# Kernel tuning notes

Measured on AMD Instinct MI355X. Metric: run time of the kernel, lower is better.

The kernel has to match this reference:

```python
import jax, jax.numpy as jnp
import numpy as np

N, E, IN, H, ED = 50000, 800000, 128, 128, 3
EPS = 1e-5

def _gat_conv(x, src, dst, ea, W, a_src, a_dst, We, a_edge, bias):
    n = x.shape[0]
    # add self loops; self-loop edge_attr = per-feature mean (PyG fill_value='mean')
    loops = jnp.arange(n, dtype=src.dtype)
    s = jnp.concatenate([src, loops])
    d = jnp.concatenate([dst, loops])
    ea_full = jnp.concatenate([ea, jnp.broadcast_to(ea.mean(0), (n, ea.shape[1]))], 0)
    h = x @ W                       # [n, H]
    al_s = h @ a_src                # [n]
    al_d = h @ a_dst
    al_e = (ea_full @ We) @ a_edge  # [E+n]
    alpha = jax.nn.leaky_relu(al_s[s] + al_d[d] + al_e, 0.2)
    # segment softmax over destination nodes (every node has a self loop)
    amax = jax.ops.segment_max(alpha, d, num_segments=n)
    ex = jnp.exp(alpha - amax[d])
    denom = jax.ops.segment_sum(ex, d, num_segments=n)
    coef = ex / (denom[d] + 1e-16)
    out = jax.ops.segment_sum(h[s] * coef[:, None], d, num_segments=n)
    return out + bias

def _bn(x, gamma, beta):
    mu = x.mean(0)
    var = ((x - mu) ** 2).mean(0)
    return (x - mu) * jax.lax.rsqrt(var + EPS) * gamma + beta

def setup_inputs():
    key = jax.random.key(0)
    ks = jax.random.split(key, 40)
    inp = {
        "x": jax.random.normal(ks[0], (N, IN), jnp.float32),
        "edge_index": jax.random.randint(ks[1], (2, E), 0, N, dtype=jnp.int32),
        "batch": jnp.zeros((N,), jnp.int32),
        "edge_attr": jax.random.normal(ks[2], (E, ED), jnp.float32),
    }
    i = 3
    for l, cin in ((1, IN), (2, H), (3, H)):
        s = 1.0 / np.sqrt(cin)
        inp[f"W{l}"] = jax.random.normal(ks[i], (cin, H), jnp.float32) * s; i += 1
        inp[f"as{l}"] = jax.random.normal(ks[i], (H,), jnp.float32) * 0.1; i += 1
        inp[f"ad{l}"] = jax.random.normal(ks[i], (H,), jnp.float32) * 0.1; i += 1
        inp[f"We{l}"] = jax.random.normal(ks[i], (ED, H), jnp.float32) * 0.5; i += 1
        inp[f"ae{l}"] = jax.random.normal(ks[i], (H,), jnp.float32) * 0.1; i += 1
        inp[f"b{l}"] = jnp.zeros((H,), jnp.float32)
        inp[f"g{l}"] = jnp.ones((H,), jnp.float32)
        inp[f"be{l}"] = jnp.zeros((H,), jnp.float32)
    return inp

def reference(x, edge_index, batch, edge_attr,
              W1, as1, ad1, We1, ae1, b1, g1, be1,
              W2, as2, ad2, We2, ae2, b2, g2, be2,
              W3, as3, ad3, We3, ae3, b3, g3, be3):
    src, dst = edge_index[0], edge_index[1]
    h = _gat_conv(x, src, dst, edge_attr, W1, as1, ad1, We1, ae1, b1)
    h = _bn(jax.nn.leaky_relu(h, 0.01), g1, be1)
    h = _gat_conv(h, src, dst, edge_attr, W2, as2, ad2, We2, ae2, b2)
    h = _bn(jax.nn.leaky_relu(h, 0.01), g2, be2)
    h = _gat_conv(h, src, dst, edge_attr, W3, as3, ad3, We3, ae3, b3)
    h = _bn(jax.nn.leaky_relu(h, 0.01), g3, be3)
    return h
```

## Files before the change

### kernel.cpp

```cpp
#include <hip/hip_runtime.h>
#include <hip/hip_fp16.h>
#include <math.h>


#define NB 64

typedef __attribute__((ext_vector_type(8))) short bf16x8;
typedef __attribute__((ext_vector_type(4))) float f32x4;

struct __align__(16) Edge2 { int src; int dst; unsigned e01; unsigned e2; };

__device__ __forceinline__ unsigned short f2bf(float x) {
  unsigned u = __float_as_uint(x);
  unsigned r = (u + 0x7FFFu + ((u >> 16) & 1u)) >> 16;
  return (unsigned short)r;
}
__device__ __forceinline__ float bf_lo(unsigned u) { return __uint_as_float(u << 16); }
__device__ __forceinline__ float bf_hi(unsigned u) { return __uint_as_float(u & 0xFFFF0000u); }

__global__ void k_hist_lds(const int* __restrict__ dst, const float* __restrict__ ea, int E,
                           int n, unsigned* __restrict__ hist32, float* __restrict__ ea_sum) {
  extern __shared__ unsigned cnt[];
  int nh = (n + 1) >> 1;
  for (int i = threadIdx.x; i < nh; i += blockDim.x) cnt[i] = 0u;
  __syncthreads();
  int tid = blockIdx.x * blockDim.x + threadIdx.x;
  int stride = gridDim.x * blockDim.x;
  float s0 = 0.f, s1 = 0.f, s2 = 0.f;
  for (int i = tid; i < E; i += stride) {
    int d = dst[i];
    atomicAdd(&cnt[d >> 1], 1u << ((d & 1) << 4));
    s0 += ea[i * 3 + 0]; s1 += ea[i * 3 + 1]; s2 += ea[i * 3 + 2];
  }
  for (int off = 32; off; off >>= 1) {
    s0 += __shfl_down(s0, off); s1 += __shfl_down(s1, off); s2 += __shfl_down(s2, off);
  }
  if ((threadIdx.x & 63) == 0) {
    atomicAdd(&ea_sum[0], s0); atomicAdd(&ea_sum[1], s1); atomicAdd(&ea_sum[2], s2);
  }
  __syncthreads();
  unsigned* plane = hist32 + (size_t)blockIdx.x * nh;
  for (int i = threadIdx.x; i < nh; i += blockDim.x) plane[i] = cnt[i];
}

__device__ __forceinline__ int wave_incl_scan(int x, int lane) {
  for (int off = 1; off < 64; off <<= 1) {
    int t = __shfl_up(x, off);
    if (lane >= off) x += t;
  }
  return x;
}

__global__ __launch_bounds__(1024) void k_scan_a(const unsigned* __restrict__ hist32, int n,
                                                 int* __restrict__ start,
                                                 int* __restrict__ bsum) {
  __shared__ int wsum[16];
  int t = threadIdx.x, lane = t & 63, w = t >> 6;
  int i = blockIdx.x * 1024 + t;
  int nh = (n + 1) >> 1;
  int stride2 = nh * 2;
  const unsigned short* h16 = (const unsigned short*)hist32;
  int v = 0;
  if (i < n) {
    for (int r = 0; r < NB; ++r) v += h16[(size_t)r * stride2 + i];
  }
  int x = wave_incl_scan(v, lane);
  if (lane == 63) wsum[w] = x;
  __syncthreads();
  if (w == 0 && lane < 16) {
    int s = wsum[lane];
    for (int off = 1; off < 16; off <<= 1) {
      int u = __shfl_up(s, off);
      if (lane >= off) s += u;
    }
    wsum[lane] = s;
  }
  __syncthreads();
  int woff = w ? wsum[w - 1] : 0;
  if (i < n) start[i] = x - v + woff;
  if (t == 1023) bsum[blockIdx.x] = wsum[15];
}

__global__ void k_scan_b(int* __restrict__ bsum, int nb, int* __restrict__ start, int n) {
  int lane = threadIdx.x;
  int v = (lane < nb) ? bsum[lane] : 0;
  int x = wave_incl_scan(v, lane);
  if (lane < nb) bsum[lane] = x - v;
  if (lane == nb - 1) start[n] = x;
}

__global__ void k_scan_c(int* __restrict__ start, const int* __restrict__ bsum,
                         const unsigned* __restrict__ hist32, int n,
                         int* __restrict__ cursorp) {
  int i = blockIdx.x * blockDim.x + threadIdx.x;
  if (i >= n) return;
  int nh = (n + 1) >> 1;
  int stride2 = nh * 2;
  const unsigned short* h16 = (const unsigned short*)hist32;
  int s = start[i] + bsum[i >> 10];
  start[i] = s;
  int run = s;
  for (int r = 0; r < NB; ++r) {
    cursorp[(size_t)r * n + i] = run;
    run += h16[(size_t)r * stride2 + i];
  }
}

__global__ void k_scatter_lds(const int* __restrict__ src, const int* __restrict__ dst,
                              const float* __restrict__ ea, int E, int n,
                              const int* __restrict__ cursorp, Edge2* __restrict__ edges) {
  extern __shared__ unsigned cnt[];
  int nh = (n + 1) >> 1;
  for (int i = threadIdx.x; i < nh; i += blockDim.x) cnt[i] = 0u;
  __syncthreads();
  const int* cur = cursorp + (size_t)blockIdx.x * n;
  int tid = blockIdx.x * blockDim.x + threadIdx.x;
  int stride = gridDim.x * blockDim.x;
  for (int i = tid; i < E; i += stride) {
    int d = dst[i];
    int sh = (d & 1) << 4;
    unsigned old = atomicAdd(&cnt[d >> 1], 1u << sh);
    int rank = (old >> sh) & 0xFFFF;
    int pos = cur[d] + rank;
    unsigned short h0 = __half_as_ushort(__float2half(ea[i * 3 + 0]));
    unsigned short h1 = __half_as_ushort(__float2half(ea[i * 3 + 1]));
    unsigned short h2 = __half_as_ushort(__float2half(ea[i * 3 + 2]));
    Edge2 e;
    e.src = src[i];
    e.dst = d;
    e.e01 = (unsigned)h0 | ((unsigned)h1 << 16);
    e.e2 = (unsigned)h2;
    edges[pos] = e;
  }
}

__device__ __forceinline__ void param_wave(const float* __restrict__ We,
                                           const float* __restrict__ ae,
                                           const float* __restrict__ ea_sum, float invE,
                                           float* __restrict__ P, int lane) {
  float a0 = ae[lane], a1 = ae[64 + lane];
  float p0 = We[0 * 128 + lane] * a0 + We[0 * 128 + 64 + lane] * a1;
  float p1 = We[1 * 128 + lane] * a0 + We[1 * 128 + 64 + lane] * a1;
  float p2 = We[2 * 128 + lane] * a0 + We[2 * 128 + 64 + lane] * a1;
  for (int off = 32; off; off >>= 1) {
    p0 += __shfl_down(p0, off); p1 += __shfl_down(p1, off); p2 += __shfl_down(p2, off);
  }
  if (lane == 0) {
    P[0] = p0; P[1] = p1; P[2] = p2;
    P[3] = ea_sum[0] * invE * p0 + ea_sum[1] * invE * p1 + ea_sum[2] * invE * p2;
  }
}

__global__ void k_param0(const float* __restrict__ We, const float* __restrict__ ae,
                         const float* __restrict__ ea_sum, float invE, float* __restrict__ P,
                         float* __restrict__ scale, float* __restrict__ shift,
                         float* __restrict__ colstats) {
  int t = threadIdx.x;
  if (t < 64) {
    param_wave(We, ae, ea_sum, invE, P, t);
  } else if (t < 192) {
    int c = t - 64;
    scale[c] = 1.f; shift[c] = 0.f;
    colstats[c] = 0.f; colstats[128 + c] = 0.f;
  }
}

__global__ void k_inter(const float* __restrict__ colstatsIn, const float* __restrict__ g,
                        const float* __restrict__ be, float invN,
                        float* __restrict__ scale, float* __restrict__ shift,
                        const float* __restrict__ WeN, const float* __restrict__ aeN,
                        const float* __restrict__ ea_sum, float invE, float* __restrict__ P,
                        float* __restrict__ colstats) {
  int t = threadIdx.x;
  if (t < 64) {
    param_wave(WeN, aeN, ea_sum, invE, P, t);
  } else if (t < 192) {
    int c = t - 64;
    float mu = colstatsIn[c] * invN;
    float var = colstatsIn[128 + c] * invN - mu * mu;
    var = var > 0.f ? var : 0.f;
    float sc = g[c] * rsqrtf(var + 1e-5f);
    scale[c] = sc;
    shift[c] = be[c] - mu * sc;
    colstats[c] = 0.f; colstats[128 + c] = 0.f;
  }
}

__global__ __launch_bounds__(256) void k_gemm3(
    const float* __restrict__ X, const float* __restrict__ Wm,
    const float* __restrict__ bnsc, const float* __restrict__ bnsh,
    const float* __restrict__ as, const float* __restrict__ ad,
    const float* __restrict__ P,
    unsigned* __restrict__ hb, float* __restrict__ al_s, float* __restrict__ al_d,
    float* __restrict__ es, int n) {
  __shared__ __align__(16) unsigned short wb[128 * 136];
  __shared__ __align__(16) unsigned short xb[64 * 136];
  int t = threadIdx.x;
  int lane = t & 63;
  int w = t >> 6;
  int c16 = lane & 15;
  int kq = lane >> 4;
  for (int i = t; i < 4096; i += 256) {
    int k = i >> 5, c4 = (i & 31) << 2;
    float4 v = ((const float4*)(Wm + k * 128))[i & 31];
    wb[(c4 + 0) * 136 + k] = f2bf(v.x);
    wb[(c4 + 1) * 136 + k] = f2bf(v.y);
    wb[(c4 + 2) * 136 + k] = f2bf(v.z);
    wb[(c4 + 3) * 136 + k] = f2bf(v.w);
  }
  float asv[8], adv[8];
#pragma unroll
  for (int ct = 0; ct < 8; ++ct) {
    asv[ct] = as[ct * 16 + c16];
    adv[ct] = ad[ct * 16 + c16];
  }
  float cself = P[3];
  int ntiles = (n + 63) >> 6;
  for (int tile = blockIdx.x; tile < ntiles; tile += gridDim.x) {
    int r0 = tile << 6;
    __syncthreads();
    for (int i = t; i < 2048; i += 256) {
      int row = i >> 5, c4 = i & 31;
      int g = r0 + row;
      float4 v;
      if (g < n) {
        v = ((const float4*)(X + (size_t)g * 128))[c4];
        float4 sc = ((const float4*)bnsc)[c4];
        float4 sh = ((const float4*)bnsh)[c4];
        v.x = fmaf(v.x, sc.x, sh.x); v.y = fmaf(v.y, sc.y, sh.y);
        v.z = fmaf(v.z, sc.z, sh.z); v.w = fmaf(v.w, sc.w, sh.w);
      } else { v.x = v.y = v.z = v.w = 0.f; }
      uint2 pk;
      pk.x = (unsigned)f2bf(v.x) | ((unsigned)f2bf(v.y) << 16);
      pk.y = (unsigned)f2bf(v.z) | ((unsigned)f2bf(v.w) << 16);
      *(uint2*)(xb + row * 136 + (c4 << 2)) = pk;
    }
    __syncthreads();
    const unsigned short* xr = xb + (w * 16 + c16) * 136 + kq * 8;
    bf16x8 A[4];
#pragma unroll
    for (int kb = 0; kb < 4; ++kb) A[kb] = *(const bf16x8*)(xr + kb * 32);
    f32x4 acc[8];
#pragma unroll
    for (int ct = 0; ct < 8; ++ct) {
      const unsigned short* wr = wb + (ct * 16 + c16) * 136 + kq * 8;
      f32x4 a = {0.f, 0.f, 0.f, 0.f};
#pragma unroll
      for (int kb = 0; kb < 4; ++kb) {
        bf16x8 B = *(const bf16x8*)(wr + kb * 32);
        a = __builtin_amdgcn_mfma_f32_16x16x32_bf16(A[kb], B, a, 0, 0, 0);
      }
      acc[ct] = a;
    }
#pragma unroll
    for (int r = 0; r < 4; ++r) {
      int R = kq * 4 + r;
      float pr = 0.f, pd = 0.f;
#pragma unroll
      for (int ct = 0; ct < 8; ++ct) {
        float hv = acc[ct][r];
        xb[(w * 16 + R) * 136 + ct * 16 + c16] = f2bf(hv);
        pr = fmaf(hv, asv[ct], pr);
        pd = fmaf(hv, adv[ct], pd);
      }
      for (int off = 8; off; off >>= 1) {
        pr += __shfl_xor(pr, off);
        pd += __shfl_xor(pd, off);
      }
      int g = r0 + w * 16 + R;
      if (c16 == 0 && g < n) {
        al_s[g] = pr; al_d[g] = pd;
        float a = pr + pd + cself;
        a = a > 0.f ? a : 0.2f * a;
        es[g] = __expf(a);
      }
    }
    __syncthreads();
    for (int i = lane; i < 256; i += 64) {
      int row = i >> 4, cc = i & 15;
      int g = r0 + w * 16 + row;
      if (g < n) {
        uint4 v = *(const uint4*)(xb + (w * 16 + row) * 136 + (cc << 3));
        *(uint4*)(hb + (size_t)g * 64 + (cc << 2)) = v;
      }
    }
  }
}

__global__ __launch_bounds__(256) void k_alpha3(const int4* __restrict__ edges,
                                                const float* __restrict__ al_s,
                                                const float* __restrict__ al_d,
                                                const float* __restrict__ P,
                                                int2* __restrict__ meta, int E) {
  int i = blockIdx.x * blockDim.x + threadIdx.x;
  if (i >= E) return;
  int4 ev = edges[i];
  float e0 = __half2float(__ushort_as_half((unsigned short)(ev.z & 0xFFFF)));
  float e1 = __half2float(__ushort_as_half((unsigned short)(((unsigned)ev.z) >> 16)));
  float e2 = __half2float(__ushort_as_half((unsigned short)(ev.w & 0xFFFF)));
  float a = al_s[ev.x] + al_d[ev.y] + e0 * P[0] + e1 * P[1] + e2 * P[2];
  a = a > 0.f ? a : 0.2f * a;
  int2 mv;
  mv.x = ev.x;
  mv.y = __float_as_int(__expf(a));
  meta[i] = mv;
}

__global__ __launch_bounds__(256) void k_agg9(const int2* __restrict__ meta,
                                              const int* __restrict__ start,
                                              const unsigned* __restrict__ hb,
                                              const float* __restrict__ es,
                                              const float* __restrict__ bias,
                                              float* __restrict__ y,
                                              float* __restrict__ colsum,
                                              float* __restrict__ colsumsq, int n) {
  int lane = threadIdx.x & 63;
  int w = threadIdx.x >> 6;
  int grp = lane >> 4;
  int sub = lane & 15;
  int gw = (blockIdx.x * blockDim.x + threadIdx.x) >> 6;
  int nw = (gridDim.x * blockDim.x) >> 6;
  int c0 = (sub << 3) + (grp << 1);
  float2 b2 = ((const float2*)bias)[(sub << 2) + grp];
  float s0 = 0.f, s1 = 0.f, q0 = 0.f, q1 = 0.f;

#define DO_QUAD(EB)                                                          \
  {                                                                          \
    int i0 = (EB), i1 = (EB) + 1, i2 = (EB) + 2, i3 = (EB) + 3;              \
    int2 m0 = meta[i0 < e1 ? i0 : e0];                                       \
    int2 m1 = meta[i1 < e1 ? i1 : e0];                                       \
    int2 m2 = meta[i2 < e1 ? i2 : e0];                                       \
    int2 m3 = meta[i3 < e1 ? i3 : e0];                                       \
    int r0 = i0 < e1 ? m0.x : i;                                             \
    int r1 = i1 < e1 ? m1.x : i;                                             \
    int r2 = i2 < e1 ? m2.x : i;                                             \
    int r3 = i3 < e1 ? m3.x : i;                                             \
    float p0 = i0 < e1 ? __int_as_float(m0.y) : 0.f;                         \
    float p1 = i1 < e1 ? __int_as_float(m1.y) : 0.f;                         \
    float p2 = i2 < e1 ? __int_as_float(m2.y) : 0.f;                         \
    float p3 = i3 < e1 ? __int_as_float(m3.y) : 0.f;                         \
    int rr = grp == 0 ? r0 : grp == 1 ? r1 : grp == 2 ? r2 : r3;             \
    float pp = grp == 0 ? p0 : grp == 1 ? p1 : grp == 2 ? p2 : p3;           \
    uint4 gv = *(const uint4*)(hb + (size_t)rr * 64 + (sub << 2));           \
    pacc += (p0 + p1) + (p2 + p3);                                           \
    aL0 = fmaf(pp, bf_lo(gv.x), aL0); aH0 = fmaf(pp, bf_hi(gv.x), aH0);      \
    aL1 = fmaf(pp, bf_lo(gv.y), aL1); aH1 = fmaf(pp, bf_hi(gv.y), aH1);      \
    aL2 = fmaf(pp, bf_lo(gv.z), aL2); aH2 = fmaf(pp, bf_hi(gv.z), aH2);      \
    aL3 = fmaf(pp, bf_lo(gv.w), aL3); aH3 = fmaf(pp, bf_hi(gv.w), aH3);      \
  }

  for (int i = gw; i < n; i += nw) {
    int e0 = __builtin_amdgcn_readfirstlane(start[i]);
    int e1 = __builtin_amdgcn_readfirstlane(start[i + 1]);
    float eself = es[i];
    uint4 hv = *(const uint4*)(hb + (size_t)i * 64 + (sub << 2));
    float wself = (grp == 0) ? eself : 0.f;
    float aL0 = wself * bf_lo(hv.x), aH0 = wself * bf_hi(hv.x);
    float aL1 = wself * bf_lo(hv.y), aH1 = wself * bf_hi(hv.y);
    float aL2 = wself * bf_lo(hv.z), aH2 = wself * bf_hi(hv.z);
    float aL3 = wself * bf_lo(hv.w), aH3 = wself * bf_hi(hv.w);
    float pacc = 0.f;
    int e = e0;
    for (; e + 8 <= e1; e += 8) {
      DO_QUAD(e);
      DO_QUAD(e + 4);
    }
    for (; e < e1; e += 4) DO_QUAD(e);
    aL0 += __shfl_xor(aL0, 16); aL0 += __shfl_xor(aL0, 32);
    aH0 += __shfl_xor(aH0, 16); aH0 += __shfl_xor(aH0, 32);
    aL1 += __shfl_xor(aL1, 16); aL1 += __shfl_xor(aL1, 32);
    aH1 += __shfl_xor(aH1, 16); aH1 += __shfl_xor(aH1, 32);
    aL2 += __shfl_xor(aL2, 16); aL2 += __shfl_xor(aL2, 32);
    aH2 += __shfl_xor(aH2, 16); aH2 += __shfl_xor(aH2, 32);
    aL3 += __shfl_xor(aL3, 16); aL3 += __shfl_xor(aL3, 32);
    aH3 += __shfl_xor(aH3, 16); aH3 += __shfl_xor(aH3, 32);
    float inv = 1.0f / (eself + pacc + 1e-16f);
    float o0 = grp == 0 ? aL0 : grp == 1 ? aL1 : grp == 2 ? aL2 : aL3;
    float o1 = grp == 0 ? aH0 : grp == 1 ? aH1 : grp == 2 ? aH2 : aH3;
    o0 = fmaf(o0, inv, b2.x);
    o1 = fmaf(o1, inv, b2.y);
    o0 = o0 > 0.f ? o0 : 0.01f * o0;
    o1 = o1 > 0.f ? o1 : 0.01f * o1;
    float2 o2 = {o0, o1};
    *(float2*)(y + (size_t)i * 128 + c0) = o2;
    s0 += o0; s1 += o1;
    q0 = fmaf(o0, o0, q0); q1 = fmaf(o1, o1, q1);
  }
#undef DO_QUAD
  __shared__ float red[4][4][64];
  red[0][w][lane] = s0; red[1][w][lane] = s1; red[2][w][lane] = q0; red[3][w][lane] = q1;
  __syncthreads();
  if (w == 0) {
    for (int ww = 1; ww < 4; ++ww) {
      s0 += red[0][ww][lane]; s1 += red[1][ww][lane];
      q0 += red[2][ww][lane]; q1 += red[3][ww][lane];
    }
    atomicAdd(&colsum[c0], s0);
    atomicAdd(&colsum[c0 + 1], s1);
    atomicAdd(&colsumsq[c0], q0);
    atomicAdd(&colsumsq[c0 + 1], q1);
  }
}

__global__ __launch_bounds__(256) void k_bnapply_final(
    const float4* __restrict__ yin, const float* __restrict__ colstats,
    const float* __restrict__ g, const float* __restrict__ be, float invN,
    float4* __restrict__ yout, int total4) {
  __shared__ float sc_s[128], sh_s[128];
  int t = threadIdx.x;
  if (t < 128) {
    float mu = colstats[t] * invN;
    float var = colstats[128 + t] * invN - mu * mu;
    var = var > 0.f ? var : 0.f;
    float sc = g[t] * rsqrtf(var + 1e-5f);
    sc_s[t] = sc;
    sh_s[t] = be[t] - mu * sc;
  }
  __syncthreads();
  for (int i = blockIdx.x * blockDim.x + t; i < total4; i += gridDim.x * blockDim.x) {
    int c4 = (i & 31) << 2;
    float4 v = yin[i];
    v.x = fmaf(v.x, sc_s[c4 + 0], sh_s[c4 + 0]);
    v.y = fmaf(v.y, sc_s[c4 + 1], sh_s[c4 + 1]);
    v.z = fmaf(v.z, sc_s[c4 + 2], sh_s[c4 + 2]);
    v.w = fmaf(v.w, sc_s[c4 + 3], sh_s[c4 + 3]);
    yout[i] = v;
  }
}

extern "C" void kernel_launch(void* const* d_in, const int* in_sizes, int n_in,
                              void* d_out, int out_size, void* d_ws, size_t ws_size,
                              hipStream_t stream) {
  const float* x = (const float*)d_in[0];
  const int* eidx = (const int*)d_in[1];
  const float* ea = (const float*)d_in[3];
  const int H = 128;
  const int N = in_sizes[0] / H;
  const int E = in_sizes[1] / 2;
  const int* srcIdx = eidx;
  const int* dstIdx = eidx + E;
  const int nh = (N + 1) >> 1;

  char* ws = (char*)d_ws;
  size_t off = 0;
  auto alloc = [&](size_t bytes) -> void* {
    void* p = ws + off;
    off = (off + bytes + 255) & ~(size_t)255;
    return p;
  };
  Edge2* edges = (Edge2*)alloc((size_t)E * sizeof(Edge2));
  int2* meta = (int2*)alloc((size_t)E * sizeof(int2));
  unsigned* hb = (unsigned*)alloc((size_t)N * 64 * sizeof(unsigned));
  float* y = (float*)alloc((size_t)N * H * sizeof(float));
  float* al_s = (float*)alloc((size_t)N * sizeof(float));
  float* al_d = (float*)alloc((size_t)N * sizeof(float));
  float* es = (float*)alloc((size_t)N * sizeof(float));
  unsigned* hist32 = (unsigned*)alloc((size_t)NB * nh * sizeof(unsigned));
  int* cursorp = (int*)alloc((size_t)NB * N * sizeof(int));
  int* start = (int*)alloc((size_t)(N + 1) * sizeof(int));
  int* bsum = (int*)alloc(64 * sizeof(int));
  float* colstats = (float*)alloc(256 * sizeof(float));
  float* colsum = colstats;
  float* colsumsq = colstats + 128;
  float* scale = (float*)alloc(128 * sizeof(float));
  float* shift = (float*)alloc(128 * sizeof(float));
  float* ea_sum = (float*)alloc(64 * sizeof(float));
  float* P = (float*)alloc(16 * sizeof(float));

  const int nb = (N + 1023) / 1024;
  const float invE = 1.0f / (float)E;
  const float invN = 1.0f / (float)N;
  const size_t ldsBytes = (size_t)nh * sizeof(unsigned);

  hipMemsetAsync(ea_sum, 0, 64 * sizeof(float), stream);
  k_hist_lds<<<NB, 256, ldsBytes, stream>>>(dstIdx, ea, E, N, hist32, ea_sum);
  k_scan_a<<<nb, 1024, 0, stream>>>(hist32, N, start, bsum);
  k_scan_b<<<1, 64, 0, stream>>>(bsum, nb, start, N);
  k_scan_c<<<(N + 255) / 256, 256, 0, stream>>>(start, bsum, hist32, N, cursorp);
  k_scatter_lds<<<NB, 256, ldsBytes, stream>>>(srcIdx, dstIdx, ea, E, N, cursorp, edges);

  const float* Wl[3]; const float* asl[3]; const float* adl[3]; const float* Wel[3];
  const float* ael[3]; const float* bl[3]; const float* gl[3]; const float* bel[3];
  for (int l = 0; l < 3; ++l) {
    Wl[l] = (const float*)d_in[4 + 8 * l + 0];
    asl[l] = (const float*)d_in[4 + 8 * l + 1];
    adl[l] = (const float*)d_in[4 + 8 * l + 2];
    Wel[l] = (const float*)d_in[4 + 8 * l + 3];
    ael[l] = (const float*)d_in[4 + 8 * l + 4];
    bl[l] = (const float*)d_in[4 + 8 * l + 5];
    gl[l] = (const float*)d_in[4 + 8 * l + 6];
    bel[l] = (const float*)d_in[4 + 8 * l + 7];
  }

  k_param0<<<1, 192, 0, stream>>>(Wel[0], ael[0], ea_sum, invE, P, scale, shift, colstats);

  const float* X = x;
  for (int l = 0; l < 3; ++l) {
    k_gemm3<<<512, 256, 0, stream>>>(X, Wl[l], scale, shift, asl[l], adl[l], P,
                                     hb, al_s, al_d, es, N);
    k_alpha3<<<(E + 255) / 256, 256, 0, stream>>>((const int4*)edges, al_s, al_d, P,
                                                  meta, E);
    k_agg9<<<2048, 256, 0, stream>>>(meta, start, hb, es, bl[l], y,
                                     colsum, colsumsq, N);
    if (l < 2) {
      k_inter<<<1, 192, 0, stream>>>(colstats, gl[l], bel[l], invN, scale, shift,
                                     Wel[l + 1], ael[l + 1], ea_sum, invE, P, colstats);
    }
    X = y;
  }
  k_bnapply_final<<<384, 256, 0, stream>>>((const float4*)y, colstats, gl[2], bel[2], invN,
                                           (float4*)d_out, N * 32);
}
```

Baseline: 722.1 us.

## Precompute per-layer edge logits at scatter time and fuse alpha into aggregation

All three layers' edge-attribute projections are now computed once in a single param kernel. The scatter kernel writes three per-layer (src, edge-logit) arrays in CSR order instead of a packed edge record. The separate per-layer alpha kernel is removed: aggregation gathers al_s[src], adds al_d and the precomputed edge term, then applies leaky-relu and exp inline. This drops one edge-sized pass per layer and its meta write/read, at the cost of three meta arrays written upfront and gathers plus exp moved into the aggregation loop.

```diff
diff --git a/kernel.cpp b/kernel.cpp
--- a/kernel.cpp
+++ b/kernel.cpp
@@ -7,8 +7,6 @@
 
 typedef __attribute__((ext_vector_type(8))) short bf16x8;
 typedef __attribute__((ext_vector_type(4))) float f32x4;
-
-struct __align__(16) Edge2 { int src; int dst; unsigned e01; unsigned e2; };
 
 __device__ __forceinline__ unsigned short f2bf(float x) {
   unsigned u = __float_as_uint(x);
@@ -108,11 +106,17 @@
 
 __global__ void k_scatter_lds(const int* __restrict__ src, const int* __restrict__ dst,
                               const float* __restrict__ ea, int E, int n,
-                              const int* __restrict__ cursorp, Edge2* __restrict__ edges) {
+                              const int* __restrict__ cursorp,
+                              const float* __restrict__ P_all,
+                              int2* __restrict__ m0a, int2* __restrict__ m1a,
+                              int2* __restrict__ m2a) {
   extern __shared__ unsigned cnt[];
   int nh = (n + 1) >> 1;
   for (int i = threadIdx.x; i < nh; i += blockDim.x) cnt[i] = 0u;
   __syncthreads();
+  float P00 = P_all[0], P01 = P_all[1], P02 = P_all[2];
+  float P10 = P_all[4], P11 = P_all[5], P12 = P_all[6];
+  float P20 = P_all[8], P21 = P_all[9], P22 = P_all[10];
   const int* cur = cursorp + (size_t)blockIdx.x * n;
   int tid = blockIdx.x * blockDim.x + threadIdx.x;
   int stride = gridDim.x * blockDim.x;
@@ -122,15 +126,16 @@
     unsigned old = atomicAdd(&cnt[d >> 1], 1u << sh);
     int rank = (old >> sh) & 0xFFFF;
     int pos = cur[d] + rank;
-    unsigned short h0 = __half_as_ushort(__float2half(ea[i * 3 + 0]));
-    unsigned short h1 = __half_as_ushort(__float2half(ea[i * 3 + 1]));
-    unsigned short h2 = __half_as_ushort(__float2half(ea[i * 3 + 2]));
-    Edge2 e;
-    e.src = src[i];
-    e.dst = d;
-    e.e01 = (unsigned)h0 | ((unsigned)h1 << 16);
-    e.e2 = (unsigned)h2;
-    edges[pos] = e;
+    float e0 = ea[i * 3 + 0], e1 = ea[i * 3 + 1], e2 = ea[i * 3 + 2];
+    int s = src[i];
+    int2 r;
+    r.x = s;
+    r.y = __float_as_int(e0 * P00 + e1 * P01 + e2 * P02);
+    m0a[pos] = r;
+    r.y = __float_as_int(e0 * P10 + e1 * P11 + e2 * P12);
+    m1a[pos] = r;
+    r.y = __float_as_int(e0 * P20 + e1 * P21 + e2 * P22);
+    m2a[pos] = r;
   }
 }
 
@@ -151,39 +156,36 @@
   }
 }
 
-__global__ void k_param0(const float* __restrict__ We, const float* __restrict__ ae,
-                         const float* __restrict__ ea_sum, float invE, float* __restrict__ P,
-                         float* __restrict__ scale, float* __restrict__ shift,
-                         float* __restrict__ colstats) {
+__global__ void k_param_all(const float* __restrict__ We0, const float* __restrict__ ae0,
+                            const float* __restrict__ We1, const float* __restrict__ ae1,
+                            const float* __restrict__ We2, const float* __restrict__ ae2,
+                            const float* __restrict__ ea_sum, float invE,
+                            float* __restrict__ P_all, float* __restrict__ scale,
+                            float* __restrict__ shift, float* __restrict__ colstats) {
   int t = threadIdx.x;
-  if (t < 64) {
-    param_wave(We, ae, ea_sum, invE, P, t);
-  } else if (t < 192) {
-    int c = t - 64;
+  if (t < 192) {
+    int l = t >> 6, lane = t & 63;
+    const float* We = l == 0 ? We0 : l == 1 ? We1 : We2;
+    const float* ae = l == 0 ? ae0 : l == 1 ? ae1 : ae2;
+    param_wave(We, ae, ea_sum, invE, P_all + 4 * l, lane);
+  } else if (t < 320) {
+    int c = t - 192;
     scale[c] = 1.f; shift[c] = 0.f;
     colstats[c] = 0.f; colstats[128 + c] = 0.f;
   }
 }
 
-__global__ void k_inter(const float* __restrict__ colstatsIn, const float* __restrict__ g,
-                        const float* __restrict__ be, float invN,
-                        float* __restrict__ scale, float* __restrict__ shift,
-                        const float* __restrict__ WeN, const float* __restrict__ aeN,
-                        const float* __restrict__ ea_sum, float invE, float* __restrict__ P,
-                        float* __restrict__ colstats) {
-  int t = threadIdx.x;
-  if (t < 64) {
-    param_wave(WeN, aeN, ea_sum, invE, P, t);
-  } else if (t < 192) {
-    int c = t - 64;
-    float mu = colstatsIn[c] * invN;
-    float var = colstatsIn[128 + c] * invN - mu * mu;
-    var = var > 0.f ? var : 0.f;
-    float sc = g[c] * rsqrtf(var + 1e-5f);
-    scale[c] = sc;
-    shift[c] = be[c] - mu * sc;
-    colstats[c] = 0.f; colstats[128 + c] = 0.f;
-  }
+__global__ void k_inter2(const float* __restrict__ g, const float* __restrict__ be,
+                         float invN, float* __restrict__ scale, float* __restrict__ shift,
+                         float* __restrict__ colstats) {
+  int c = threadIdx.x;
+  float mu = colstats[c] * invN;
+  float var = colstats[128 + c] * invN - mu * mu;
+  var = var > 0.f ? var : 0.f;
+  float sc = g[c] * rsqrtf(var + 1e-5f);
+  scale[c] = sc;
+  shift[c] = be[c] - mu * sc;
+  colstats[c] = 0.f; colstats[128 + c] = 0.f;
 }
 
 __global__ __launch_bounds__(256) void k_gemm3(
@@ -287,33 +289,16 @@
   }
 }
 
-__global__ __launch_bounds__(256) void k_alpha3(const int4* __restrict__ edges,
-                                                const float* __restrict__ al_s,
-                                                const float* __restrict__ al_d,
-                                                const float* __restrict__ P,
-                                                int2* __restrict__ meta, int E) {
-  int i = blockIdx.x * blockDim.x + threadIdx.x;
-  if (i >= E) return;
-  int4 ev = edges[i];
-  float e0 = __half2float(__ushort_as_half((unsigned short)(ev.z & 0xFFFF)));
-  float e1 = __half2float(__ushort_as_half((unsigned short)(((unsigned)ev.z) >> 16)));
-  float e2 = __half2float(__ushort_as_half((unsigned short)(ev.w & 0xFFFF)));
-  float a = al_s[ev.x] + al_d[ev.y] + e0 * P[0] + e1 * P[1] + e2 * P[2];
-  a = a > 0.f ? a : 0.2f * a;
-  int2 mv;
-  mv.x = ev.x;
-  mv.y = __float_as_int(__expf(a));
-  meta[i] = mv;
-}
-
-__global__ __launch_bounds__(256) void k_agg9(const int2* __restrict__ meta,
-                                              const int* __restrict__ start,
-                                              const unsigned* __restrict__ hb,
-                                              const float* __restrict__ es,
-                                              const float* __restrict__ bias,
-                                              float* __restrict__ y,
-                                              float* __restrict__ colsum,
-                                              float* __restrict__ colsumsq, int n) {
+__global__ __launch_bounds__(256) void k_agg11(const int2* __restrict__ meta,
+                                               const int* __restrict__ start,
+                                               const unsigned* __restrict__ hb,
+                                               const float* __restrict__ es,
+                                               const float* __restrict__ al_s,
+                                               const float* __restrict__ al_d,
+                                               const float* __restrict__ bias,
+                                               float* __restrict__ y,
+                                               float* __restrict__ colsum,
+                                               float* __restrict__ colsumsq, int n) {
   int lane = threadIdx.x & 63;
   int w = threadIdx.x >> 6;
   int grp = lane >> 4;
@@ -335,10 +320,18 @@
     int r1 = i1 < e1 ? m1.x : i;                                             \
     int r2 = i2 < e1 ? m2.x : i;                                             \
     int r3 = i3 < e1 ? m3.x : i;                                             \
-    float p0 = i0 < e1 ? __int_as_float(m0.y) : 0.f;                         \
-    float p1 = i1 < e1 ? __int_as_float(m1.y) : 0.f;                         \
-    float p2 = i2 < e1 ? __int_as_float(m2.y) : 0.f;                         \
-    float p3 = i3 < e1 ? __int_as_float(m3.y) : 0.f;                         \
+    float a0 = al_s[r0] + ad_i + __int_as_float(m0.y);                       \
+    float a1 = al_s[r1] + ad_i + __int_as_float(m1.y);                       \
+    float a2 = al_s[r2] + ad_i + __int_as_float(m2.y);                       \
+    float a3 = al_s[r3] + ad_i + __int_as_float(m3.y);                       \
+    a0 = a0 > 0.f ? a0 : 0.2f * a0;                                          \
+    a1 = a1 > 0.f ? a1 : 0.2f * a1;                                          \
+    a2 = a2 > 0.f ? a2 : 0.2f * a2;                                          \
+    a3 = a3 > 0.f ? a3 : 0.2f * a3;                                          \
+    float p0 = i0 < e1 ? __expf(a0) : 0.f;                                   \
+    float p1 = i1 < e1 ? __expf(a1) : 0.f;                                   \
+    float p2 = i2 < e1 ? __expf(a2) : 0.f;                                   \
+    float p3 = i3 < e1 ? __expf(a3) : 0.f;                                   \
     int rr = grp == 0 ? r0 : grp == 1 ? r1 : grp == 2 ? r2 : r3;             \
     float pp = grp == 0 ? p0 : grp == 1 ? p1 : grp == 2 ? p2 : p3;           \
     uint4 gv = *(const uint4*)(hb + (size_t)rr * 64 + (sub << 2));           \
@@ -353,6 +346,7 @@
     int e0 = __builtin_amdgcn_readfirstlane(start[i]);
     int e1 = __builtin_amdgcn_readfirstlane(start[i + 1]);
     float eself = es[i];
+    float ad_i = al_d[i];
     uint4 hv = *(const uint4*)(hb + (size_t)i * 64 + (sub << 2));
     float wself = (grp == 0) ? eself : 0.f;
     float aL0 = wself * bf_lo(hv.x), aH0 = wself * bf_hi(hv.x);
@@ -448,8 +442,9 @@
     off = (off + bytes + 255) & ~(size_t)255;
     return p;
   };
-  Edge2* edges = (Edge2*)alloc((size_t)E * sizeof(Edge2));
-  int2* meta = (int2*)alloc((size_t)E * sizeof(int2));
+  int2* meta0 = (int2*)alloc((size_t)E * sizeof(int2));
+  int2* meta1 = (int2*)alloc((size_t)E * sizeof(int2));
+  int2* meta2 = (int2*)alloc((size_t)E * sizeof(int2));
   unsigned* hb = (unsigned*)alloc((size_t)N * 64 * sizeof(unsigned));
   float* y = (float*)alloc((size_t)N * H * sizeof(float));
   float* al_s = (float*)alloc((size_t)N * sizeof(float));
@@ -465,19 +460,12 @@
   float* scale = (float*)alloc(128 * sizeof(float));
   float* shift = (float*)alloc(128 * sizeof(float));
   float* ea_sum = (float*)alloc(64 * sizeof(float));
-  float* P = (float*)alloc(16 * sizeof(float));
+  float* P_all = (float*)alloc(16 * sizeof(float));
 
   const int nb = (N + 1023) / 1024;
   const float invE = 1.0f / (float)E;
   const float invN = 1.0f / (float)N;
   const size_t ldsBytes = (size_t)nh * sizeof(unsigned);
-
-  hipMemsetAsync(ea_sum, 0, 64 * sizeof(float), stream);
-  k_hist_lds<<<NB, 256, ldsBytes, stream>>>(dstIdx, ea, E, N, hist32, ea_sum);
-  k_scan_a<<<nb, 1024, 0, stream>>>(hist32, N, start, bsum);
-  k_scan_b<<<1, 64, 0, stream>>>(bsum, nb, start, N);
-  k_scan_c<<<(N + 255) / 256, 256, 0, stream>>>(start, bsum, hist32, N, cursorp);
-  k_scatter_lds<<<NB, 256, ldsBytes, stream>>>(srcIdx, dstIdx, ea, E, N, cursorp, edges);
 
   const float* Wl[3]; const float* asl[3]; const float* adl[3]; const float* Wel[3];
   const float* ael[3]; const float* bl[3]; const float* gl[3]; const float* bel[3];
@@ -492,19 +480,25 @@
     bel[l] = (const float*)d_in[4 + 8 * l + 7];
   }
 
-  k_param0<<<1, 192, 0, stream>>>(Wel[0], ael[0], ea_sum, invE, P, scale, shift, colstats);
-
+  hipMemsetAsync(ea_sum, 0, 64 * sizeof(float), stream);
+  k_hist_lds<<<NB, 256, ldsBytes, stream>>>(dstIdx, ea, E, N, hist32, ea_sum);
+  k_param_all<<<1, 320, 0, stream>>>(Wel[0], ael[0], Wel[1], ael[1], Wel[2], ael[2],
+                                     ea_sum, invE, P_all, scale, shift, colstats);
+  k_scan_a<<<nb, 1024, 0, stream>>>(hist32, N, start, bsum);
+  k_scan_b<<<1, 64, 0, stream>>>(bsum, nb, start, N);
+  k_scan_c<<<(N + 255) / 256, 256, 0, stream>>>(start, bsum, hist32, N, cursorp);
+  k_scatter_lds<<<NB, 256, ldsBytes, stream>>>(srcIdx, dstIdx, ea, E, N, cursorp,
+                                               P_all, meta0, meta1, meta2);
+
+  int2* metas[3] = {meta0, meta1, meta2};
   const float* X = x;
   for (int l = 0; l < 3; ++l) {
-    k_gemm3<<<512, 256, 0, stream>>>(X, Wl[l], scale, shift, asl[l], adl[l], P,
-                                     hb, al_s, al_d, es, N);
-    k_alpha3<<<(E + 255) / 256, 256, 0, stream>>>((const int4*)edges, al_s, al_d, P,
-                                                  meta, E);
-    k_agg9<<<2048, 256, 0, stream>>>(meta, start, hb, es, bl[l], y,
-                                     colsum, colsumsq, N);
+    k_gemm3<<<512, 256, 0, stream>>>(X, Wl[l], scale, shift, asl[l], adl[l],
+                                     P_all + 4 * l, hb, al_s, al_d, es, N);
+    k_agg11<<<2048, 256, 0, stream>>>(metas[l], start, hb, es, al_s, al_d, bl[l], y,
+                                      colsum, colsumsq, N);
     if (l < 2) {
-      k_inter<<<1, 192, 0, stream>>>(colstats, gl[l], bel[l], invN, scale, shift,
-                                     Wel[l + 1], ael[l + 1], ea_sum, invE, P, colstats);
+      k_inter2<<<1, 128, 0, stream>>>(gl[l], bel[l], invN, scale, shift, colstats);
     }
     X = y;
   }
```

Result: faster. 694.3 us (-3.9%).
